# Optimization experiments

Hardware: AMD Instinct MI355X
Metric: run time of the kernel (lower is better)

## Reference

```python
import jax, jax.numpy as jnp
import numpy as np

SEQ, BATCH, IN = 512, 256, 15
H1, H2, FC_HID, NUM_CLASSES = 512, 512, 64, 1


def setup_inputs() -> dict:
    key = jax.random.key(0)
    ks = jax.random.split(key, 14)
    def u(k, shape, fan_in):
        b = 1.0 / np.sqrt(fan_in)
        return jax.random.uniform(k, shape, jnp.float32, -b, b)
    return {
        "x": jax.random.normal(ks[0], (SEQ, BATCH, IN), jnp.float32),
        # PyTorch LSTM params, gate order i,f,g,o stacked along dim 0
        "W_ih1": u(ks[1], (4 * H1, IN), H1),
        "W_hh1": u(ks[2], (4 * H1, H1), H1),
        "b_ih1": u(ks[3], (4 * H1,), H1),
        "b_hh1": u(ks[4], (4 * H1,), H1),
        "W_ih2": u(ks[5], (4 * H2, H1), H2),
        "W_hh2": u(ks[6], (4 * H2, H2), H2),
        "b_ih2": u(ks[7], (4 * H2,), H2),
        "b_hh2": u(ks[8], (4 * H2,), H2),
        "fc1_w": u(ks[9], (FC_HID, H2), H2),
        "fc1_b": u(ks[10], (FC_HID,), H2),
        "fc_w": u(ks[11], (NUM_CLASSES, FC_HID), FC_HID),
        "fc_b": u(ks[12], (NUM_CLASSES,), FC_HID),
    }


def _lstm_cell(x_t, h, c, W_ih, W_hh, b_ih, b_hh):
    # gates: [B, 4H], PyTorch gate order i, f, g, o
    g = x_t @ W_ih.T + b_ih + h @ W_hh.T + b_hh
    i, f, gg, o = jnp.split(g, 4, axis=-1)
    c_new = jax.nn.sigmoid(f) * c + jax.nn.sigmoid(i) * jnp.tanh(gg)
    h_new = jax.nn.sigmoid(o) * jnp.tanh(c_new)
    return h_new, c_new


def reference(x, W_ih1, W_hh1, b_ih1, b_hh1, W_ih2, W_hh2, b_ih2, b_hh2,
              fc1_w, fc1_b, fc_w, fc_b):
    S, B, _ = x.shape
    init = (jnp.zeros((B, H1), x.dtype), jnp.zeros((B, H1), x.dtype),
            jnp.zeros((B, H2), x.dtype), jnp.zeros((B, H2), x.dtype))

    def step(carry, x_t):
        h1, c1, h2, c2 = carry
        h1, c1 = _lstm_cell(x_t, h1, c1, W_ih1, W_hh1, b_ih1, b_hh1)
        h2, c2 = _lstm_cell(h1, h2, c2, W_ih2, W_hh2, b_ih2, b_hh2)
        return (h1, c1, h2, c2), None

    (h1, c1, h2, c2), _ = jax.lax.scan(step, init, x)
    # MLP head on final-timestep top-layer hidden state; `out += out` doubles it
    hn = jax.nn.relu(h2)
    out = jax.nn.relu(hn @ fc1_w.T + fc1_b)
    out = out @ fc_w.T + fc_b
    return out + out
```

## Files before the change

### kernel.cpp

```cpp
#include <hip/hip_runtime.h>
#include <cstdint>
#include <cstddef>

typedef __attribute__((ext_vector_type(8))) short short8;
typedef __attribute__((ext_vector_type(4))) float floatx4;

constexpr int kSeq = 512;
constexpr int kBatch = 256;
constexpr int kIn = 15;
constexpr int kH = 512;
constexpr int kG = 4 * kH;
constexpr int kRing = 17;
constexpr size_t kHSlot = (size_t)kBatch * kH;
constexpr size_t kShmemBytes = 131072 + 4096;

__device__ __forceinline__ unsigned short f2bf(float f) {
    union { float f; unsigned u; } v; v.f = f;
    unsigned u = v.u;
    return (unsigned short)((u + 0x7fffu + ((u >> 16) & 1u)) >> 16);
}

__device__ __forceinline__ float sigm(float x) { return 1.0f / (1.0f + __expf(-x)); }
__device__ __forceinline__ float tanh_(float x) { return 1.0f - 2.0f / (1.0f + __expf(2.0f * x)); }

#define LLC_STORE16(P, V)                                                     \
    asm volatile("global_store_dwordx4 %0, %1, off sc0 sc1"                   \
                 :: "v"(P), "v"(V) : "memory")

__device__ __forceinline__ void waitf(const int* flags, int tgt, int lane, int& fc) {
    if (tgt <= 0) return;
    bool watch = (lane < 32);
    if (__all(!watch || fc >= tgt)) return;
    int spin = 0;
    for (;;) {
        if (watch && fc < tgt)
            fc = __hip_atomic_load(flags + lane * 16,
                                   __ATOMIC_RELAXED, __HIP_MEMORY_SCOPE_AGENT);
        if (__all(!watch || fc >= tgt)) return;
        if (++spin > 4096) __builtin_amdgcn_s_sleep(8);
    }
}

__global__ void k_conv(const float* __restrict__ src, unsigned short* __restrict__ dst, int n) {
    int i = blockIdx.x * blockDim.x + threadIdx.x;
    if (i < n) dst[i] = f2bf(src[i]);
}

__global__ void k_conv_pad(const float* __restrict__ src, unsigned short* __restrict__ dst, int rows) {
    int i = blockIdx.x * blockDim.x + threadIdx.x;
    if (i >= rows * 32) return;
    int r = i >> 5, k = i & 31;
    dst[i] = (k < kIn) ? f2bf(src[r * kIn + k]) : (unsigned short)0;
}

__global__ __launch_bounds__(256) void k_persist(
    const unsigned short* __restrict__ whh1b,
    const unsigned short* __restrict__ wih1b,
    const unsigned short* __restrict__ wih2b,
    const unsigned short* __restrict__ whh2b,
    const unsigned short* __restrict__ xb,
    const float* __restrict__ bih1, const float* __restrict__ bhh1,
    const float* __restrict__ bih2, const float* __restrict__ bhh2,
    unsigned short* __restrict__ h1r,
    unsigned short* __restrict__ h2r,
    float* __restrict__ h2f,
    int* __restrict__ flags)
{
    extern __shared__ unsigned short lw[];
    const int bid = blockIdx.x;
    const int g = bid & 3;
    const int role = bid >> 2;
    const bool is2 = role >= 32;
    const int rid = role & 31;
    const int j0 = rid << 4;
    const int tid = (int)threadIdx.x;
    const int wave = tid >> 6;
    const int lane = tid & 63;
    const int lcol = lane & 15;
    const int quad = lane >> 4;
    const int m0 = (g << 6) + wave * 16;
    const int arow = m0 + lcol;
    const int koff = quad * 8;

    int* f1 = flags + g * 1024;
    int* f2 = f1 + 512;
    int* myflag = (is2 ? f2 : f1) + rid * 16;
    unsigned short* scr = lw + 65536 + wave * 384;

    if (!is2) {
        for (int i = tid; i < 4096; i += 256) {
            int ln = i >> 6, gg = ln >> 4, u = ln & 15;
            int c = i & 63, kk = c >> 2, qd = c & 3;
            *(short8*)&lw[((gg * 16 + kk) << 9) + ((qd * 16 + u) << 3)] =
                *(const short8*)&whh1b[(size_t)((gg << 9) + j0 + u) * kH + c * 8];
        }
        for (int i = tid; i < 256; i += 256) {
            int ln = i >> 2, gg = ln >> 4, u = ln & 15;
            int qd = i & 3;
            *(short8*)&lw[((64 + gg) << 9) + ((qd * 16 + u) << 3)] =
                *(const short8*)&wih1b[((gg << 9) + j0 + u) * 32 + qd * 8];
        }
    } else {
        for (int i = tid; i < 4096; i += 256) {
            int ln = i >> 6, gg = ln >> 4, u = ln & 15;
            int c = i & 63, kk = c >> 2, qd = c & 3;
            int dst = ((gg * 16 + kk) << 9) + ((qd * 16 + u) << 3);
            size_t src = (size_t)((gg << 9) + j0 + u) * kH + c * 8;
            *(short8*)&lw[dst] = *(const short8*)&wih2b[src];
            *(short8*)&lw[dst + (64 << 9)] = *(const short8*)&whh2b[src];
        }
    }
    float bsum[4];
#pragma unroll
    for (int gg = 0; gg < 4; ++gg) {
        int n = (gg << 9) + j0 + lcol;
        bsum[gg] = is2 ? (bih2[n] + bhh2[n]) : (bih1[n] + bhh1[n]);
    }
    __syncthreads();

    float creg[4] = {0.f, 0.f, 0.f, 0.f};
    int fc1 = 0, fc2 = 0;

    if (!is2) {
        for (int s = 0; s < kSeq; ++s) {
            if ((s & 15) == 0) {
                waitf(f1, s, lane, fc1);
                waitf(f2, s, lane, fc2);
                __builtin_amdgcn_fence(__ATOMIC_ACQUIRE, "agent");
            }
            floatx4 acc[4];
#pragma unroll
            for (int gg = 0; gg < 4; ++gg)
                acc[gg] = (floatx4){bsum[gg], bsum[gg], bsum[gg], bsum[gg]};

            short8 ax = *(const short8*)(xb + ((size_t)s * kBatch + arow) * 32 + koff);

            waitf(f1, s, lane, fc1);
            const unsigned short* hp = h1r + (size_t)((s + 16) % kRing) * kHSlot
                                       + (size_t)arow * kH + koff;
            short8 a[16];
#pragma unroll
            for (int kk = 0; kk < 16; ++kk) a[kk] = *(const short8*)(hp + kk * 32);
#pragma unroll
            for (int kk = 0; kk < 16; ++kk) {
#pragma unroll
                for (int gg = 0; gg < 4; ++gg) {
                    short8 b = *(const short8*)&lw[((gg * 16 + kk) << 9) + (lane << 3)];
                    acc[gg] = __builtin_amdgcn_mfma_f32_16x16x32_bf16(a[kk], b, acc[gg], 0, 0, 0);
                }
            }
#pragma unroll
            for (int gg = 0; gg < 4; ++gg) {
                short8 b = *(const short8*)&lw[((64 + gg) << 9) + (lane << 3)];
                acc[gg] = __builtin_amdgcn_mfma_f32_16x16x32_bf16(ax, b, acc[gg], 0, 0, 0);
            }

            unsigned short* hw = h1r + (size_t)(s % kRing) * kHSlot;
#pragma unroll
            for (int r = 0; r < 4; ++r) {
                int row = quad * 4 + r;
                float gi = acc[0][r], gf = acc[1][r], ggv = acc[2][r], go = acc[3][r];
                float cn = sigm(gf) * creg[r] + sigm(gi) * tanh_(ggv);
                float hn = sigm(go) * tanh_(cn);
                creg[r] = cn;
                scr[row * 24 + lcol] = f2bf(hn);
            }
            if (lane < 32) {
                int row = lane >> 1, seg = lane & 1;
                short8 v = *(short8*)&scr[row * 24 + seg * 8];
                unsigned short* gp = hw + (size_t)(m0 + row) * kH + j0 + seg * 8;
                LLC_STORE16(gp, v);
            }
            __builtin_amdgcn_s_waitcnt(0);
            __syncthreads();
            if (tid == 0)
                __hip_atomic_store(myflag, s + 1,
                                   __ATOMIC_RELAXED, __HIP_MEMORY_SCOPE_AGENT);
        }
    } else {
        for (int u = 0; u < kSeq; ++u) {
            if ((u & 15) == 0) {
                waitf(f1, u, lane, fc1);
                waitf(f2, u, lane, fc2);
                __builtin_amdgcn_fence(__ATOMIC_ACQUIRE, "agent");
            }
            floatx4 acc[4];
#pragma unroll
            for (int gg = 0; gg < 4; ++gg)
                acc[gg] = (floatx4){bsum[gg], bsum[gg], bsum[gg], bsum[gg]};

            waitf(f2, u, lane, fc2);

            const unsigned short* hp2 = h2r + (size_t)((u + 16) % kRing) * kHSlot
                                        + (size_t)arow * kH + koff;
            short8 a[16];
#pragma unroll
            for (int kk = 0; kk < 16; ++kk) a[kk] = *(const short8*)(hp2 + kk * 32);
#pragma unroll
            for (int kk = 0; kk < 16; ++kk) {
#pragma unroll
                for (int gg = 0; gg < 4; ++gg) {
                    short8 b = *(const short8*)&lw[((64 + gg * 16 + kk) << 9) + (lane << 3)];
                    acc[gg] = __builtin_amdgcn_mfma_f32_16x16x32_bf16(a[kk], b, acc[gg], 0, 0, 0);
                }
            }

            waitf(f1, u + 1, lane, fc1);

            const unsigned short* hp1 = h1r + (size_t)(u % kRing) * kHSlot
                                        + (size_t)arow * kH + koff;
#pragma unroll
            for (int kk = 0; kk < 16; ++kk) a[kk] = *(const short8*)(hp1 + kk * 32);
#pragma unroll
            for (int kk = 0; kk < 16; ++kk) {
#pragma unroll
                for (int gg = 0; gg < 4; ++gg) {
                    short8 b = *(const short8*)&lw[((gg * 16 + kk) << 9) + (lane << 3)];
                    acc[gg] = __builtin_amdgcn_mfma_f32_16x16x32_bf16(a[kk], b, acc[gg], 0, 0, 0);
                }
            }

            unsigned short* hw = h2r + (size_t)(u % kRing) * kHSlot;
            const int j = j0 + lcol;
#pragma unroll
            for (int r = 0; r < 4; ++r) {
                int row = quad * 4 + r;
                float gi = acc[0][r], gf = acc[1][r], ggv = acc[2][r], go = acc[3][r];
                float cn = sigm(gf) * creg[r] + sigm(gi) * tanh_(ggv);
                float hn = sigm(go) * tanh_(cn);
                creg[r] = cn;
                scr[row * 24 + lcol] = f2bf(hn);
                if (u == kSeq - 1) h2f[(size_t)(m0 + row) * kH + j] = hn;
            }
            if (lane < 32) {
                int row = lane >> 1, seg = lane & 1;
                short8 v = *(short8*)&scr[row * 24 + seg * 8];
                unsigned short* gp = hw + (size_t)(m0 + row) * kH + j0 + seg * 8;
                LLC_STORE16(gp, v);
            }
            __builtin_amdgcn_s_waitcnt(0);
            __syncthreads();
            if (tid == 0)
                __hip_atomic_store(myflag, u + 1,
                                   __ATOMIC_RELAXED, __HIP_MEMORY_SCOPE_AGENT);
        }
    }
}

__global__ __launch_bounds__(64) void k_head(
    const float* __restrict__ h2f, const float* __restrict__ fc1w,
    const float* __restrict__ fc1b, const float* __restrict__ fcw,
    const float* __restrict__ fcb, float* __restrict__ out)
{
    int m = blockIdx.x;
    int j = threadIdx.x;
    const float* hr = h2f + (size_t)m * kH;
    const float* wr = fc1w + (size_t)j * kH;
    float sacc = 0.f;
    for (int k = 0; k < kH; ++k) sacc += fmaxf(hr[k], 0.f) * wr[k];
    float rv = fmaxf(sacc + fc1b[j], 0.f) * fcw[j];
#pragma unroll
    for (int off = 32; off >= 1; off >>= 1) rv += __shfl_down(rv, off);
    if (j == 0) out[m] = 2.0f * (rv + fcb[0]);
}

extern "C" void kernel_launch(void* const* d_in, const int* in_sizes, int n_in,
                              void* d_out, int out_size, void* d_ws, size_t ws_size,
                              hipStream_t stream) {
    const float* x    = (const float*)d_in[0];
    const float* Wih1 = (const float*)d_in[1];
    const float* Whh1 = (const float*)d_in[2];
    const float* bih1 = (const float*)d_in[3];
    const float* bhh1 = (const float*)d_in[4];
    const float* Wih2 = (const float*)d_in[5];
    const float* Whh2 = (const float*)d_in[6];
    const float* bih2 = (const float*)d_in[7];
    const float* bhh2 = (const float*)d_in[8];
    const float* fc1w = (const float*)d_in[9];
    const float* fc1b = (const float*)d_in[10];
    const float* fcw  = (const float*)d_in[11];
    const float* fcb  = (const float*)d_in[12];
    float* out = (float*)d_out;

    char* p = (char*)d_ws;
    auto take = [&](size_t bytes) -> char* {
        char* r = p;
        p += (bytes + 255) & ~(size_t)255;
        return r;
    };
    unsigned short* whh1b = (unsigned short*)take((size_t)kG * kH * 2);
    unsigned short* wih2b = (unsigned short*)take((size_t)kG * kH * 2);
    unsigned short* whh2b = (unsigned short*)take((size_t)kG * kH * 2);
    unsigned short* wih1b = (unsigned short*)take((size_t)kG * 32 * 2);
    unsigned short* xb    = (unsigned short*)take((size_t)kSeq * kBatch * 32 * 2);
    char* state = p;
    unsigned short* h1r = (unsigned short*)take((size_t)kRing * kHSlot * 2);
    unsigned short* h2r = (unsigned short*)take((size_t)kRing * kHSlot * 2);
    int* flags = (int*)take(16384);
    size_t state_bytes = (size_t)((char*)flags + 16384 - state);
    float* h2f = (float*)take((size_t)kBatch * kH * 4);

    hipMemsetAsync(state, 0, state_bytes, stream);

    int n = kG * kH;
    k_conv<<<(n + 255) / 256, 256, 0, stream>>>(Whh1, whh1b, n);
    k_conv<<<(n + 255) / 256, 256, 0, stream>>>(Wih2, wih2b, n);
    k_conv<<<(n + 255) / 256, 256, 0, stream>>>(Whh2, whh2b, n);
    k_conv_pad<<<(kG * 32 + 255) / 256, 256, 0, stream>>>(Wih1, wih1b, kG);
    k_conv_pad<<<(kSeq * kBatch * 32 + 255) / 256, 256, 0, stream>>>(x, xb, kSeq * kBatch);

    hipFuncSetAttribute((const void*)k_persist,
                        hipFuncAttributeMaxDynamicSharedMemorySize, (int)kShmemBytes);
    void* args[] = {&whh1b, &wih1b, &wih2b, &whh2b, &xb,
                    (void*)&bih1, (void*)&bhh1, (void*)&bih2, (void*)&bhh2,
                    &h1r, &h2r, &h2f, &flags};
    hipError_t e = hipLaunchCooperativeKernel((const void*)k_persist, dim3(256), dim3(256),
                                              args, (unsigned)kShmemBytes, stream);
    if (e != hipSuccess) {
        k_persist<<<256, 256, kShmemBytes, stream>>>(
            whh1b, wih1b, wih2b, whh2b, xb, bih1, bhh1, bih2, bhh2,
            h1r, h2r, h2f, flags);
    }

    k_head<<<kBatch, 64, 0, stream>>>(h2f, fc1w, fc1b, fcw, fcb, out);
}
```

Before: 4.164 ms.

## Fuse both LSTM layers into each block and halve persistent grid

```diff
diff --git a/kernel.cpp b/kernel.cpp
--- a/kernel.cpp
+++ b/kernel.cpp
@@ -12,7 +12,7 @@
 constexpr int kG = 4 * kH;
 constexpr int kRing = 17;
 constexpr size_t kHSlot = (size_t)kBatch * kH;
-constexpr size_t kShmemBytes = 131072 + 4096;
+constexpr size_t kShmemBytes = 141312;
 
 __device__ __forceinline__ unsigned short f2bf(float f) {
     union { float f; unsigned u; } v; v.f = f;
@@ -29,14 +29,11 @@
 
 __device__ __forceinline__ void waitf(const int* flags, int tgt, int lane, int& fc) {
     if (tgt <= 0) return;
-    bool watch = (lane < 32);
-    if (__all(!watch || fc >= tgt)) return;
+    const int* myf = flags + (lane & 31) * 16;
     int spin = 0;
-    for (;;) {
-        if (watch && fc < tgt)
-            fc = __hip_atomic_load(flags + lane * 16,
-                                   __ATOMIC_RELAXED, __HIP_MEMORY_SCOPE_AGENT);
-        if (__all(!watch || fc >= tgt)) return;
+    while (!__all(fc >= tgt)) {
+        if (fc < tgt)
+            fc = __hip_atomic_load(myf, __ATOMIC_RELAXED, __HIP_MEMORY_SCOPE_AGENT);
         if (++spin > 4096) __builtin_amdgcn_s_sleep(8);
     }
 }
@@ -69,9 +66,7 @@
     extern __shared__ unsigned short lw[];
     const int bid = blockIdx.x;
     const int g = bid & 3;
-    const int role = bid >> 2;
-    const bool is2 = role >= 32;
-    const int rid = role & 31;
+    const int rid = bid >> 2;
     const int j0 = rid << 4;
     const int tid = (int)threadIdx.x;
     const int wave = tid >> 6;
@@ -82,166 +77,171 @@
     const int arow = m0 + lcol;
     const int koff = quad * 8;
 
-    int* f1 = flags + g * 1024;
-    int* f2 = f1 + 512;
-    int* myflag = (is2 ? f2 : f1) + rid * 16;
-    unsigned short* scr = lw + 65536 + wave * 384;
-
-    if (!is2) {
-        for (int i = tid; i < 4096; i += 256) {
-            int ln = i >> 6, gg = ln >> 4, u = ln & 15;
-            int c = i & 63, kk = c >> 2, qd = c & 3;
-            *(short8*)&lw[((gg * 16 + kk) << 9) + ((qd * 16 + u) << 3)] =
-                *(const short8*)&whh1b[(size_t)((gg << 9) + j0 + u) * kH + c * 8];
-        }
-        for (int i = tid; i < 256; i += 256) {
-            int ln = i >> 2, gg = ln >> 4, u = ln & 15;
-            int qd = i & 3;
-            *(short8*)&lw[((64 + gg) << 9) + ((qd * 16 + u) << 3)] =
-                *(const short8*)&wih1b[((gg << 9) + j0 + u) * 32 + qd * 8];
-        }
-    } else {
-        for (int i = tid; i < 4096; i += 256) {
-            int ln = i >> 6, gg = ln >> 4, u = ln & 15;
-            int c = i & 63, kk = c >> 2, qd = c & 3;
-            int dst = ((gg * 16 + kk) << 9) + ((qd * 16 + u) << 3);
-            size_t src = (size_t)((gg << 9) + j0 + u) * kH + c * 8;
-            *(short8*)&lw[dst] = *(const short8*)&wih2b[src];
-            *(short8*)&lw[dst + (64 << 9)] = *(const short8*)&whh2b[src];
-        }
-    }
-    float bsum[4];
+    int* f = flags + g * 512;
+    int* myflag = f + rid * 16;
+    unsigned short* scr = lw + 67584 + wave * 768;
+
+    for (int i = tid; i < 4096; i += 256) {
+        int ln = i >> 6, gg = ln >> 4, u = ln & 15;
+        int c = i & 63, kk = c >> 2, qd = c & 3;
+        int dst = ((gg * 16 + kk) << 9) + ((qd * 16 + u) << 3);
+        size_t src = (size_t)((gg << 9) + j0 + u) * kH + c * 8;
+        *(short8*)&lw[dst] = *(const short8*)&whh1b[src];
+        *(short8*)&lw[dst + (68 << 9)] = *(const short8*)&whh2b[src];
+    }
+    for (int i = tid; i < 256; i += 256) {
+        int ln = i >> 2, gg = ln >> 4, u = ln & 15;
+        int qd = i & 3;
+        *(short8*)&lw[((64 + gg) << 9) + ((qd * 16 + u) << 3)] =
+            *(const short8*)&wih1b[((gg << 9) + j0 + u) * 32 + qd * 8];
+    }
+    float bsum1[4], bsum2[4];
 #pragma unroll
     for (int gg = 0; gg < 4; ++gg) {
         int n = (gg << 9) + j0 + lcol;
-        bsum[gg] = is2 ? (bih2[n] + bhh2[n]) : (bih1[n] + bhh1[n]);
-    }
+        bsum1[gg] = bih1[n] + bhh1[n];
+        bsum2[gg] = bih2[n] + bhh2[n];
+    }
+    const unsigned short* wstream = wih2b + (size_t)(j0 + lcol) * kH + koff;
     __syncthreads();
 
-    float creg[4] = {0.f, 0.f, 0.f, 0.f};
-    int fc1 = 0, fc2 = 0;
-
-    if (!is2) {
-        for (int s = 0; s < kSeq; ++s) {
-            if ((s & 15) == 0) {
-                waitf(f1, s, lane, fc1);
-                waitf(f2, s, lane, fc2);
-                __builtin_amdgcn_fence(__ATOMIC_ACQUIRE, "agent");
-            }
-            floatx4 acc[4];
+    float creg1[4] = {0.f, 0.f, 0.f, 0.f};
+    float creg2[4] = {0.f, 0.f, 0.f, 0.f};
+    int fc = 0;
+
+    {
+        floatx4 acc[4];
+#pragma unroll
+        for (int gg = 0; gg < 4; ++gg)
+            acc[gg] = (floatx4){bsum1[gg], bsum1[gg], bsum1[gg], bsum1[gg]};
+        short8 ax = *(const short8*)(xb + (size_t)arow * 32 + koff);
+#pragma unroll
+        for (int gg = 0; gg < 4; ++gg) {
+            short8 b = *(const short8*)&lw[((64 + gg) << 9) + (lane << 3)];
+            acc[gg] = __builtin_amdgcn_mfma_f32_16x16x32_bf16(ax, b, acc[gg], 0, 0, 0);
+        }
+        unsigned short* hw = h1r + (size_t)16 * kHSlot;
+#pragma unroll
+        for (int r = 0; r < 4; ++r) {
+            int row = quad * 4 + r;
+            float gi = acc[0][r], gf = acc[1][r], gv = acc[2][r], go = acc[3][r];
+            float cn = sigm(gf) * creg1[r] + sigm(gi) * tanh_(gv);
+            float hn = sigm(go) * tanh_(cn);
+            creg1[r] = cn;
+            scr[384 + row * 24 + lcol] = f2bf(hn);
+        }
+        if (lane < 32) {
+            int row = lane >> 1, seg = lane & 1;
+            short8 v = *(short8*)&scr[384 + row * 24 + seg * 8];
+            unsigned short* gp = hw + (size_t)(m0 + row) * kH + j0 + seg * 8;
+            LLC_STORE16(gp, v);
+        }
+        __builtin_amdgcn_s_waitcnt(0);
+        __syncthreads();
+        if (tid == 0)
+            __hip_atomic_store(myflag, 1, __ATOMIC_RELAXED, __HIP_MEMORY_SCOPE_AGENT);
+    }
+
+    for (int t = 0; t < kSeq; ++t) {
+        waitf(f, t + 1, lane, fc);
+        if ((t & 15) == 0)
+            __builtin_amdgcn_fence(__ATOMIC_ACQUIRE, "agent");
+
+        const int sr = (t + 16) % kRing;
+        const int sw = t % kRing;
+        const unsigned short* hp1 = h1r + (size_t)sr * kHSlot + (size_t)arow * kH + koff;
+        const unsigned short* hp2 = h2r + (size_t)sr * kHSlot + (size_t)arow * kH + koff;
+        short8 a1[16], a2[16];
+#pragma unroll
+        for (int kk = 0; kk < 16; ++kk) a2[kk] = *(const short8*)(hp2 + kk * 32);
+#pragma unroll
+        for (int kk = 0; kk < 16; ++kk) a1[kk] = *(const short8*)(hp1 + kk * 32);
+
+        floatx4 acc2[4];
+#pragma unroll
+        for (int gg = 0; gg < 4; ++gg)
+            acc2[gg] = (floatx4){bsum2[gg], bsum2[gg], bsum2[gg], bsum2[gg]};
+
+#pragma unroll
+        for (int kk = 0; kk < 16; ++kk) {
+#pragma unroll
+            for (int gg = 0; gg < 4; ++gg) {
+                short8 b = *(const short8*)&lw[((68 + gg * 16 + kk) << 9) + (lane << 3)];
+                acc2[gg] = __builtin_amdgcn_mfma_f32_16x16x32_bf16(a2[kk], b, acc2[gg], 0, 0, 0);
+            }
+        }
+#pragma unroll
+        for (int gg = 0; gg < 4; ++gg) {
+            const unsigned short* wp = wstream + (size_t)gg * (512 * 512);
+            short8 bfr[16];
+#pragma unroll
+            for (int kk = 0; kk < 16; ++kk) bfr[kk] = *(const short8*)(wp + kk * 32);
+#pragma unroll
+            for (int kk = 0; kk < 16; ++kk)
+                acc2[gg] = __builtin_amdgcn_mfma_f32_16x16x32_bf16(a1[kk], bfr[kk], acc2[gg], 0, 0, 0);
+        }
+
+        floatx4 acc1[4];
+        if (t < kSeq - 1) {
 #pragma unroll
             for (int gg = 0; gg < 4; ++gg)
-                acc[gg] = (floatx4){bsum[gg], bsum[gg], bsum[gg], bsum[gg]};
-
-            short8 ax = *(const short8*)(xb + ((size_t)s * kBatch + arow) * 32 + koff);
-
-            waitf(f1, s, lane, fc1);
-            const unsigned short* hp = h1r + (size_t)((s + 16) % kRing) * kHSlot
-                                       + (size_t)arow * kH + koff;
-            short8 a[16];
-#pragma unroll
-            for (int kk = 0; kk < 16; ++kk) a[kk] = *(const short8*)(hp + kk * 32);
+                acc1[gg] = (floatx4){bsum1[gg], bsum1[gg], bsum1[gg], bsum1[gg]};
+            short8 ax = *(const short8*)(xb + ((size_t)(t + 1) * kBatch + arow) * 32 + koff);
 #pragma unroll
             for (int kk = 0; kk < 16; ++kk) {
 #pragma unroll
                 for (int gg = 0; gg < 4; ++gg) {
                     short8 b = *(const short8*)&lw[((gg * 16 + kk) << 9) + (lane << 3)];
-                    acc[gg] = __builtin_amdgcn_mfma_f32_16x16x32_bf16(a[kk], b, acc[gg], 0, 0, 0);
+                    acc1[gg] = __builtin_amdgcn_mfma_f32_16x16x32_bf16(a1[kk], b, acc1[gg], 0, 0, 0);
                 }
             }
 #pragma unroll
             for (int gg = 0; gg < 4; ++gg) {
                 short8 b = *(const short8*)&lw[((64 + gg) << 9) + (lane << 3)];
-                acc[gg] = __builtin_amdgcn_mfma_f32_16x16x32_bf16(ax, b, acc[gg], 0, 0, 0);
-            }
-
-            unsigned short* hw = h1r + (size_t)(s % kRing) * kHSlot;
+                acc1[gg] = __builtin_amdgcn_mfma_f32_16x16x32_bf16(ax, b, acc1[gg], 0, 0, 0);
+            }
+        }
+
+        unsigned short* hw2 = h2r + (size_t)sw * kHSlot;
+        const int j = j0 + lcol;
+#pragma unroll
+        for (int r = 0; r < 4; ++r) {
+            int row = quad * 4 + r;
+            float gi = acc2[0][r], gf = acc2[1][r], gv = acc2[2][r], go = acc2[3][r];
+            float cn = sigm(gf) * creg2[r] + sigm(gi) * tanh_(gv);
+            float hn = sigm(go) * tanh_(cn);
+            creg2[r] = cn;
+            scr[row * 24 + lcol] = f2bf(hn);
+            if (t == kSeq - 1) h2f[(size_t)(m0 + row) * kH + j] = hn;
+        }
+        unsigned short* hw1 = h1r + (size_t)sw * kHSlot;
+        if (t < kSeq - 1) {
 #pragma unroll
             for (int r = 0; r < 4; ++r) {
                 int row = quad * 4 + r;
-                float gi = acc[0][r], gf = acc[1][r], ggv = acc[2][r], go = acc[3][r];
-                float cn = sigm(gf) * creg[r] + sigm(gi) * tanh_(ggv);
+                float gi = acc1[0][r], gf = acc1[1][r], gv = acc1[2][r], go = acc1[3][r];
+                float cn = sigm(gf) * creg1[r] + sigm(gi) * tanh_(gv);
                 float hn = sigm(go) * tanh_(cn);
-                creg[r] = cn;
-                scr[row * 24 + lcol] = f2bf(hn);
-            }
-            if (lane < 32) {
-                int row = lane >> 1, seg = lane & 1;
-                short8 v = *(short8*)&scr[row * 24 + seg * 8];
-                unsigned short* gp = hw + (size_t)(m0 + row) * kH + j0 + seg * 8;
-                LLC_STORE16(gp, v);
-            }
+                creg1[r] = cn;
+                scr[384 + row * 24 + lcol] = f2bf(hn);
+            }
+        }
+        if (lane < 32) {
+            int row = lane >> 1, seg = lane & 1;
+            short8 v2 = *(short8*)&scr[row * 24 + seg * 8];
+            unsigned short* gp2 = hw2 + (size_t)(m0 + row) * kH + j0 + seg * 8;
+            LLC_STORE16(gp2, v2);
+            if (t < kSeq - 1) {
+                short8 v1 = *(short8*)&scr[384 + row * 24 + seg * 8];
+                unsigned short* gp1 = hw1 + (size_t)(m0 + row) * kH + j0 + seg * 8;
+                LLC_STORE16(gp1, v1);
+            }
+        }
+        if (t < kSeq - 1) {
             __builtin_amdgcn_s_waitcnt(0);
             __syncthreads();
             if (tid == 0)
-                __hip_atomic_store(myflag, s + 1,
-                                   __ATOMIC_RELAXED, __HIP_MEMORY_SCOPE_AGENT);
-        }
-    } else {
-        for (int u = 0; u < kSeq; ++u) {
-            if ((u & 15) == 0) {
-                waitf(f1, u, lane, fc1);
-                waitf(f2, u, lane, fc2);
-                __builtin_amdgcn_fence(__ATOMIC_ACQUIRE, "agent");
-            }
-            floatx4 acc[4];
-#pragma unroll
-            for (int gg = 0; gg < 4; ++gg)
-                acc[gg] = (floatx4){bsum[gg], bsum[gg], bsum[gg], bsum[gg]};
-
-            waitf(f2, u, lane, fc2);
-
-            const unsigned short* hp2 = h2r + (size_t)((u + 16) % kRing) * kHSlot
-                                        + (size_t)arow * kH + koff;
-            short8 a[16];
-#pragma unroll
-            for (int kk = 0; kk < 16; ++kk) a[kk] = *(const short8*)(hp2 + kk * 32);
-#pragma unroll
-            for (int kk = 0; kk < 16; ++kk) {
-#pragma unroll
-                for (int gg = 0; gg < 4; ++gg) {
-                    short8 b = *(const short8*)&lw[((64 + gg * 16 + kk) << 9) + (lane << 3)];
-                    acc[gg] = __builtin_amdgcn_mfma_f32_16x16x32_bf16(a[kk], b, acc[gg], 0, 0, 0);
-                }
-            }
-
-            waitf(f1, u + 1, lane, fc1);
-
-            const unsigned short* hp1 = h1r + (size_t)(u % kRing) * kHSlot
-                                        + (size_t)arow * kH + koff;
-#pragma unroll
-            for (int kk = 0; kk < 16; ++kk) a[kk] = *(const short8*)(hp1 + kk * 32);
-#pragma unroll
-            for (int kk = 0; kk < 16; ++kk) {
-#pragma unroll
-                for (int gg = 0; gg < 4; ++gg) {
-                    short8 b = *(const short8*)&lw[((gg * 16 + kk) << 9) + (lane << 3)];
-                    acc[gg] = __builtin_amdgcn_mfma_f32_16x16x32_bf16(a[kk], b, acc[gg], 0, 0, 0);
-                }
-            }
-
-            unsigned short* hw = h2r + (size_t)(u % kRing) * kHSlot;
-            const int j = j0 + lcol;
-#pragma unroll
-            for (int r = 0; r < 4; ++r) {
-                int row = quad * 4 + r;
-                float gi = acc[0][r], gf = acc[1][r], ggv = acc[2][r], go = acc[3][r];
-                float cn = sigm(gf) * creg[r] + sigm(gi) * tanh_(ggv);
-                float hn = sigm(go) * tanh_(cn);
-                creg[r] = cn;
-                scr[row * 24 + lcol] = f2bf(hn);
-                if (u == kSeq - 1) h2f[(size_t)(m0 + row) * kH + j] = hn;
-            }
-            if (lane < 32) {
-                int row = lane >> 1, seg = lane & 1;
-                short8 v = *(short8*)&scr[row * 24 + seg * 8];
-                unsigned short* gp = hw + (size_t)(m0 + row) * kH + j0 + seg * 8;
-                LLC_STORE16(gp, v);
-            }
-            __builtin_amdgcn_s_waitcnt(0);
-            __syncthreads();
-            if (tid == 0)
-                __hip_atomic_store(myflag, u + 1,
+                __hip_atomic_store(myflag, t + 2,
                                    __ATOMIC_RELAXED, __HIP_MEMORY_SCOPE_AGENT);
         }
     }
@@ -314,10 +314,10 @@
     void* args[] = {&whh1b, &wih1b, &wih2b, &whh2b, &xb,
                     (void*)&bih1, (void*)&bhh1, (void*)&bih2, (void*)&bhh2,
                     &h1r, &h2r, &h2f, &flags};
-    hipError_t e = hipLaunchCooperativeKernel((const void*)k_persist, dim3(256), dim3(256),
+    hipError_t e = hipLaunchCooperativeKernel((const void*)k_persist, dim3(128), dim3(256),
                                               args, (unsigned)kShmemBytes, stream);
     if (e != hipSuccess) {
-        k_persist<<<256, 256, kShmemBytes, stream>>>(
+        k_persist<<<128, 256, kShmemBytes, stream>>>(
             whh1b, wih1b, wih2b, whh2b, xb, bih1, bhh1, bih2, bhh2,
             h1r, h2r, h2f, flags);
     }
```

After: 5.489 ms. +31.8%, slower.
